# Optimization experiments

Measured on AMD Instinct MI355X. Metric: run time of the kernel, lower is better.

## Reference

```python
import jax, jax.numpy as jnp
import numpy as np

N = 100000        # nodes in the batched graph
E = 1_600_000     # directed edges
G = 256           # graphs in the batch
IN, H = 3, 64
EPS = 1e-5        # BatchNorm eps (eval mode: running stats, dropout off)


def setup_inputs() -> dict:
    key = jax.random.key(0)
    ks = jax.random.split(key, 40)
    inp = {}
    inp["x"] = jax.random.normal(ks[0], (N, IN), jnp.float32)
    inp["edge_index"] = jax.random.randint(ks[1], (2, E), 0, N, dtype=jnp.int32)
    inp["batch_idx"] = jnp.sort(jax.random.randint(ks[2], (N,), 0, G, dtype=jnp.int32))
    dims = [IN, H, H, H]  # zip(dims[:-1], dims[1:]) -> 3 GCN layers (as in source)
    k = 3
    for i in range(3):
        inp[f"W{i}"] = jax.random.normal(ks[k], (dims[i], dims[i + 1]), jnp.float32) * 0.1; k += 1
        inp[f"b{i}"] = jax.random.normal(ks[k], (dims[i + 1],), jnp.float32) * 0.01; k += 1
        inp[f"g{i}"] = jax.random.uniform(ks[k], (dims[i + 1],), jnp.float32, 0.5, 1.5); k += 1
        inp[f"be{i}"] = jax.random.normal(ks[k], (dims[i + 1],), jnp.float32) * 0.1; k += 1
        inp[f"rm{i}"] = jax.random.normal(ks[k], (dims[i + 1],), jnp.float32) * 0.1; k += 1
        inp[f"rv{i}"] = jax.random.uniform(ks[k], (dims[i + 1],), jnp.float32, 0.5, 1.5); k += 1
    inp["mW1"] = jax.random.normal(ks[k], (2 * H, 32), jnp.float32) * 0.1; k += 1
    inp["mb1"] = jnp.zeros((32,), jnp.float32)
    inp["mW2"] = jax.random.normal(ks[k], (32, 16), jnp.float32) * 0.1; k += 1
    inp["mb2"] = jnp.zeros((16,), jnp.float32)
    inp["mW3"] = jax.random.normal(ks[k], (16, 1), jnp.float32) * 0.1; k += 1
    inp["mb3"] = jnp.zeros((1,), jnp.float32)
    return inp


def _gcn(x, W, b, src, dst):
    # PyG GCNConv: add self-loops, symmetric D^-1/2 (A+I) D^-1/2 normalization
    h = x @ W                                   # [N, out]
    deg = jnp.zeros((N,), h.dtype).at[dst].add(1.0) + 1.0  # +1 self-loop
    dinv = jax.lax.rsqrt(deg)
    coef = dinv[src] * dinv[dst]                # [E]
    agg = jax.ops.segment_sum(h[src] * coef[:, None], dst, num_segments=N)
    agg = agg + h * (dinv * dinv)[:, None]      # self-loop message
    return agg + b


def _bn(x, g, be, rm, rv):
    return (x - rm) * jax.lax.rsqrt(rv + EPS) * g + be


def _forward(x, edge_index, batch_idx,
             W0, b0, g0, be0, rm0, rv0,
             W1, b1, g1, be1, rm1, rv1,
             W2, b2, g2, be2, rm2, rv2,
             mW1, mb1, mW2, mb2, mW3, mb3):
    src, dst = edge_index[0], edge_index[1]
    layers = [(W0, b0, g0, be0, rm0, rv0), (W1, b1, g1, be1, rm1, rv1), (W2, b2, g2, be2, rm2, rv2)]
    for (W, b, g, be, rm, rv) in layers:
        x = jax.nn.relu(_bn(_gcn(x, W, b, src, dst), g, be, rm, rv))
    cnt = jax.ops.segment_sum(jnp.ones((N,), x.dtype), batch_idx, num_segments=G)
    x_mean = jax.ops.segment_sum(x, batch_idx, num_segments=G) / jnp.maximum(cnt, 1.0)[:, None]
    x_max = jax.ops.segment_max(x, batch_idx, num_segments=G)
    x_max = jnp.where(jnp.isfinite(x_max), x_max, 0.0)
    xg = jnp.concatenate([x_mean, x_max], axis=1)  # [G, 2H]
    h = jax.nn.relu(xg @ mW1 + mb1)
    h = jax.nn.relu(h @ mW2 + mb2)
    return h @ mW3 + mb3                            # [G, 1]


def reference(x, edge_index, batch_idx,
              W0, b0, g0, be0, rm0, rv0,
              W1, b1, g1, be1, rm1, rv1,
              W2, b2, g2, be2, rm2, rv2,
              mW1, mb1, mW2, mb2, mW3, mb3):
    return _forward(x, edge_index, batch_idx,
                    W0, b0, g0, be0, rm0, rv0,
                    W1, b1, g1, be1, rm1, rv1,
                    W2, b2, g2, be2, rm2, rv2,
                    mW1, mb1, mW2, mb2, mW3, mb3)
```

## Files before the change

### kernel.cpp

```cpp
#include <hip/hip_runtime.h>
#include <hip/hip_fp16.h>

#define NN 100000
#define EE 1600000
#define GG 256
#define EPS 1e-5f
#define KB2 ((NN + 511) >> 9)
#define BCAP 10240
#define EPB 4096
#define EBLK ((EE + EPB - 1) / EPB)
#define NB256 ((NN + 255) / 256)

__device__ __forceinline__ unsigned int pack2(float x, float y) {
  __half2 h = __float22half2_rn(make_float2(x, y));
  return *reinterpret_cast<unsigned int*>(&h);
}
__device__ __forceinline__ uint2 pack4(float x, float y, float z, float w) {
  uint2 r;
  r.x = pack2(x, y);
  r.y = pack2(z, w);
  return r;
}
__device__ __forceinline__ void add8(float4& a0, float4& a1, uint4 v) {
  __half2 h0 = *reinterpret_cast<__half2*>(&v.x);
  __half2 h1 = *reinterpret_cast<__half2*>(&v.y);
  __half2 h2 = *reinterpret_cast<__half2*>(&v.z);
  __half2 h3 = *reinterpret_cast<__half2*>(&v.w);
  float2 f0 = __half22float2(h0), f1 = __half22float2(h1);
  float2 f2 = __half22float2(h2), f3 = __half22float2(h3);
  a0.x += f0.x; a0.y += f0.y; a0.z += f1.x; a0.w += f1.y;
  a1.x += f2.x; a1.y += f2.y; a1.z += f3.x; a1.w += f3.y;
}

__device__ __forceinline__ void gld16(uint4& d, const uint4* p) {
  asm volatile("global_load_dwordx4 %0, %1, off" : "=v"(d) : "v"(p));
}
__device__ __forceinline__ void gldf16(float4& d, const float4* p) {
  asm volatile("global_load_dwordx4 %0, %1, off" : "=v"(d) : "v"(p));
}

__global__ void k_passA(const int* __restrict__ ei, int* __restrict__ bfill,
                        int* __restrict__ tmp) {
  __shared__ int cnt[KB2], cur[KB2], base[KB2];
  int t = threadIdx.x;
  for (int b = t; b < KB2; b += 256) { cnt[b] = 0; cur[b] = 0; }
  __syncthreads();
  int e0 = blockIdx.x * EPB;
  int myb[16], myp[16];
#pragma unroll
  for (int j = 0; j < 16; ++j) {
    int e = e0 + j * 256 + t;
    int bb = -1, pp = 0;
    if (e < EE) {
      int ss = ei[e];
      int dd = ei[EE + e];
      bb = dd >> 9;
      pp = (ss << 9) | (dd & 511);
    }
    myb[j] = bb;
    myp[j] = pp;
    if (bb >= 0) atomicAdd(&cnt[bb], 1);
  }
  __syncthreads();
  for (int b = t; b < KB2; b += 256)
    if (cnt[b] > 0) base[b] = b * BCAP + atomicAdd(&bfill[b], cnt[b]);
  __syncthreads();
#pragma unroll
  for (int j = 0; j < 16; ++j) {
    int bb = myb[j];
    if (bb >= 0) {
      int slot = base[bb] + atomicAdd(&cur[bb], 1);
      tmp[slot] = myp[j];
    }
  }
}

__global__ void k_bucket(const int* __restrict__ tmp, const int* __restrict__ bfill,
                         const float* __restrict__ x, int* __restrict__ csr,
                         int* __restrict__ row, int* __restrict__ rowe,
                         float* __restrict__ dinv, float4* __restrict__ xd) {
  __shared__ int cnt[512], s[512], fillp[512];
  __shared__ int stmp[BCAP];
  int b = blockIdx.x, t = threadIdx.x;
  int nb = b << 9;
  int e0 = b * BCAP;
  int fill = bfill[b];
  cnt[t] = 0;
  cnt[t + 256] = 0;
  for (int e = t; e < fill; e += 256) stmp[e] = tmp[e0 + e];
  __syncthreads();
  for (int e = t; e < fill; e += 256) atomicAdd(&cnt[stmp[e] & 511], 1);
  __syncthreads();
  s[t] = cnt[t];
  s[t + 256] = cnt[t + 256];
  __syncthreads();
  for (int off = 1; off < 512; off <<= 1) {
    int i1 = t + 256;
    int v0 = (t >= off) ? s[t - off] : 0;
    int v1 = (i1 >= off) ? s[i1 - off] : 0;
    __syncthreads();
    s[t] += v0;
    s[i1] += v1;
    __syncthreads();
  }
#pragma unroll
  for (int k = 0; k < 2; ++k) {
    int i = t + k * 256;
    int excl = s[i] - cnt[i];
    fillp[i] = excl;
    int dst = nb + i;
    if (dst < NN) {
      row[dst] = e0 + excl;
      rowe[dst] = e0 + s[i];
      float d = rsqrtf((float)cnt[i] + 1.0f);
      dinv[dst] = d;
      xd[dst] = make_float4(x[dst * 3] * d, x[dst * 3 + 1] * d, x[dst * 3 + 2] * d, 0.f);
    }
  }
  __syncthreads();
  for (int e = t; e < fill; e += 256) {
    int ed = stmp[e];
    int slot = atomicAdd(&fillp[ed & 511], 1);
    csr[e0 + slot] = ed >> 9;
  }
}

__launch_bounds__(256, 4)
__global__ void k_agg3f(const float4* __restrict__ xd, const int* __restrict__ row,
                        const int* __restrict__ rowe, const int* __restrict__ csr,
                        const float* __restrict__ dinv,
                        const float* __restrict__ W, const float* __restrict__ b,
                        const float* __restrict__ gam, const float* __restrict__ bet,
                        const float* __restrict__ rm, const float* __restrict__ rv,
                        uint2* __restrict__ out) {
  int n = blockIdx.x * 256 + threadIdx.x;
  if (n >= NN) return;
  int s0 = row[n], s1 = rowe[n];
  float4 a = xd[n];
  float ax = a.x, ay = a.y, az = a.z;
  for (int i = s0; i < s1; i += 16) {
    int idx[16];
#pragma unroll
    for (int j = 0; j < 16; ++j) idx[j] = csr[min(i + j, s1 - 1)];
    float4 v[16];
#pragma unroll
    for (int j = 0; j < 16; ++j) gldf16(v[j], xd + idx[j]);
    asm volatile("s_waitcnt vmcnt(0)" ::: "memory");
    __builtin_amdgcn_sched_barrier(0);
    int rem = s1 - i;
#pragma unroll
    for (int j = 0; j < 16; ++j)
      if (j < rem) { ax += v[j].x; ay += v[j].y; az += v[j].z; }
  }
  float d = dinv[n];
  float t0 = ax * d, t1 = ay * d, t2 = az * d;
  const float4* W4 = (const float4*)W;
  const float4* b4 = (const float4*)b;
  const float4* g4p = (const float4*)gam;
  const float4* be4p = (const float4*)bet;
  const float4* rm4p = (const float4*)rm;
  const float4* rv4p = (const float4*)rv;
#pragma unroll
  for (int c4 = 0; c4 < 16; ++c4) {
    float4 w0 = W4[c4], w1 = W4[16 + c4], w2 = W4[32 + c4];
    float4 bb = b4[c4], g4 = g4p[c4], be4 = be4p[c4], rm4 = rm4p[c4], rv4 = rv4p[c4];
    float4 o;
    o.x = fmaf(t0, w0.x, fmaf(t1, w1.x, fmaf(t2, w2.x, bb.x)));
    o.y = fmaf(t0, w0.y, fmaf(t1, w1.y, fmaf(t2, w2.y, bb.y)));
    o.z = fmaf(t0, w0.z, fmaf(t1, w1.z, fmaf(t2, w2.z, bb.z)));
    o.w = fmaf(t0, w0.w, fmaf(t1, w1.w, fmaf(t2, w2.w, bb.w)));
    float scx = g4.x * rsqrtf(rv4.x + EPS), shx = be4.x - rm4.x * scx;
    float scy = g4.y * rsqrtf(rv4.y + EPS), shy = be4.y - rm4.y * scy;
    float scz = g4.z * rsqrtf(rv4.z + EPS), shz = be4.z - rm4.z * scz;
    float scw = g4.w * rsqrtf(rv4.w + EPS), shw = be4.w - rm4.w * scw;
    o.x = fmaxf(fmaf(o.x, scx, shx), 0.f) * d;
    o.y = fmaxf(fmaf(o.y, scy, shy), 0.f) * d;
    o.z = fmaxf(fmaf(o.z, scz, shz), 0.f) * d;
    o.w = fmaxf(fmaf(o.w, scw, shw), 0.f) * d;
    out[(size_t)n * 16 + c4] = pack4(o.x, o.y, o.z, o.w);
  }
}

template <bool MID>
__launch_bounds__(256, 4)
__global__ void k_layer2(const uint4* __restrict__ xs, const int* __restrict__ row,
                         const int* __restrict__ rowe, const int* __restrict__ csr,
                         const float* __restrict__ dinv,
                         const float* __restrict__ W, const float* __restrict__ b,
                         const float* __restrict__ gam, const float* __restrict__ bet,
                         const float* __restrict__ rm, const float* __restrict__ rv,
                         uint4* __restrict__ outv) {
  __shared__ float sh[32][68];
  int t = blockIdx.x * 256 + threadIdx.x;
  int n = t >> 3, sub = t & 7;
  int local = threadIdx.x >> 3;
  int s0 = row[n], s1 = rowe[n];
  float4 a0 = make_float4(0.f, 0.f, 0.f, 0.f);
  float4 a1 = make_float4(0.f, 0.f, 0.f, 0.f);
  add8(a0, a1, xs[(size_t)n * 8 + sub]);
  if (s0 < s1) {
    int e = s0 + sub;
    int myidx = (e < s1) ? csr[e] : n;
    for (int i = s0; i < s1; i += 8) {
      int e2 = i + 8 + sub;
      int pre = csr[min(e2, s1 - 1)];
      uint4 v0, v1, v2, v3, v4, v5, v6, v7;
      gld16(v0, xs + ((size_t)__shfl(myidx, 0, 8) * 8 + sub));
      gld16(v1, xs + ((size_t)__shfl(myidx, 1, 8) * 8 + sub));
      gld16(v2, xs + ((size_t)__shfl(myidx, 2, 8) * 8 + sub));
      gld16(v3, xs + ((size_t)__shfl(myidx, 3, 8) * 8 + sub));
      gld16(v4, xs + ((size_t)__shfl(myidx, 4, 8) * 8 + sub));
      gld16(v5, xs + ((size_t)__shfl(myidx, 5, 8) * 8 + sub));
      gld16(v6, xs + ((size_t)__shfl(myidx, 6, 8) * 8 + sub));
      gld16(v7, xs + ((size_t)__shfl(myidx, 7, 8) * 8 + sub));
      asm volatile("s_waitcnt vmcnt(0)" ::: "memory");
      __builtin_amdgcn_sched_barrier(0);
      int rem = s1 - i;
      add8(a0, a1, v0);
      if (rem > 1) add8(a0, a1, v1);
      if (rem > 2) add8(a0, a1, v2);
      if (rem > 3) add8(a0, a1, v3);
      if (rem > 4) add8(a0, a1, v4);
      if (rem > 5) add8(a0, a1, v5);
      if (rem > 6) add8(a0, a1, v6);
      if (rem > 7) add8(a0, a1, v7);
      myidx = (e2 < s1) ? pre : n;
    }
  }
  float d = dinv[n];
  float4 w0 = make_float4(a0.x * d, a0.y * d, a0.z * d, a0.w * d);
  float4 w1 = make_float4(a1.x * d, a1.y * d, a1.z * d, a1.w * d);
  *(float4*)&sh[local][sub * 8] = w0;
  *(float4*)&sh[local][sub * 8 + 4] = w1;
  __syncthreads();
  const float4* W4 = (const float4*)W;
  float4 accA = ((const float4*)b)[sub * 2];
  float4 accB = ((const float4*)b)[sub * 2 + 1];
#pragma unroll 8
  for (int k = 0; k < 64; ++k) {
    float xv = sh[local][k];
    float4 wA = W4[k * 16 + sub * 2];
    float4 wB = W4[k * 16 + sub * 2 + 1];
    accA.x = fmaf(xv, wA.x, accA.x);
    accA.y = fmaf(xv, wA.y, accA.y);
    accA.z = fmaf(xv, wA.z, accA.z);
    accA.w = fmaf(xv, wA.w, accA.w);
    accB.x = fmaf(xv, wB.x, accB.x);
    accB.y = fmaf(xv, wB.y, accB.y);
    accB.z = fmaf(xv, wB.z, accB.z);
    accB.w = fmaf(xv, wB.w, accB.w);
  }
  float4 gA = ((const float4*)gam)[sub * 2], gB = ((const float4*)gam)[sub * 2 + 1];
  float4 beA = ((const float4*)bet)[sub * 2], beB = ((const float4*)bet)[sub * 2 + 1];
  float4 rmA = ((const float4*)rm)[sub * 2], rmB = ((const float4*)rm)[sub * 2 + 1];
  float4 rvA = ((const float4*)rv)[sub * 2], rvB = ((const float4*)rv)[sub * 2 + 1];
  float4 oA, oB;
  {
    float sc = gA.x * rsqrtf(rvA.x + EPS); oA.x = fmaxf(fmaf(accA.x, sc, beA.x - rmA.x * sc), 0.f);
    sc = gA.y * rsqrtf(rvA.y + EPS); oA.y = fmaxf(fmaf(accA.y, sc, beA.y - rmA.y * sc), 0.f);
    sc = gA.z * rsqrtf(rvA.z + EPS); oA.z = fmaxf(fmaf(accA.z, sc, beA.z - rmA.z * sc), 0.f);
    sc = gA.w * rsqrtf(rvA.w + EPS); oA.w = fmaxf(fmaf(accA.w, sc, beA.w - rmA.w * sc), 0.f);
    sc = gB.x * rsqrtf(rvB.x + EPS); oB.x = fmaxf(fmaf(accB.x, sc, beB.x - rmB.x * sc), 0.f);
    sc = gB.y * rsqrtf(rvB.y + EPS); oB.y = fmaxf(fmaf(accB.y, sc, beB.y - rmB.y * sc), 0.f);
    sc = gB.z * rsqrtf(rvB.z + EPS); oB.z = fmaxf(fmaf(accB.z, sc, beB.z - rmB.z * sc), 0.f);
    sc = gB.w * rsqrtf(rvB.w + EPS); oB.w = fmaxf(fmaf(accB.w, sc, beB.w - rmB.w * sc), 0.f);
  }
  uint4 r;
  if (MID) {
    r.x = pack2(oA.x * d, oA.y * d);
    r.y = pack2(oA.z * d, oA.w * d);
    r.z = pack2(oB.x * d, oB.y * d);
    r.w = pack2(oB.z * d, oB.w * d);
  } else {
    r.x = pack2(oA.x, oA.y);
    r.y = pack2(oA.z, oA.w);
    r.z = pack2(oB.x, oB.y);
    r.w = pack2(oB.z, oB.w);
  }
  outv[(size_t)n * 8 + sub] = r;
}

__device__ __forceinline__ int lower_bound(const int* __restrict__ b, int target) {
  int lo = 0, hi = NN;
  while (lo < hi) {
    int m = (lo + hi) >> 1;
    if (b[m] < target) lo = m + 1; else hi = m;
  }
  return lo;
}

__global__ void k_poolmlp(const uint2* __restrict__ feat, const int* __restrict__ bidx,
                          const float* __restrict__ mW1, const float* __restrict__ mb1,
                          const float* __restrict__ mW2, const float* __restrict__ mb2,
                          const float* __restrict__ mW3, const float* __restrict__ mb3,
                          float* __restrict__ out) {
  __shared__ float4 shs[64][17], shm[64][17];
  __shared__ float xg[128], h1[32], h2[16];
  int g = blockIdx.x, t = threadIdx.x;
  int c4 = t & 15, r = t >> 4;
  int lo = lower_bound(bidx, g);
  int hi = lower_bound(bidx, g + 1);
  float4 s = make_float4(0.f, 0.f, 0.f, 0.f);
  float4 m = make_float4(0.f, 0.f, 0.f, 0.f);
  for (int i = lo + r; i < hi; i += 64) {
    uint2 u = feat[(size_t)i * 16 + c4];
    __half2 h0 = *reinterpret_cast<__half2*>(&u.x);
    __half2 h1v = *reinterpret_cast<__half2*>(&u.y);
    float2 f0 = __half22float2(h0), f1 = __half22float2(h1v);
    s.x += f0.x; s.y += f0.y; s.z += f1.x; s.w += f1.y;
    m.x = fmaxf(m.x, f0.x); m.y = fmaxf(m.y, f0.y);
    m.z = fmaxf(m.z, f1.x); m.w = fmaxf(m.w, f1.y);
  }
  shs[r][c4] = s;
  shm[r][c4] = m;
  __syncthreads();
  if (t < 16) {
    float4 cs = shs[0][t], cm = shm[0][t];
#pragma unroll
    for (int r2 = 1; r2 < 64; ++r2) {
      float4 as = shs[r2][t], am = shm[r2][t];
      cs.x += as.x; cs.y += as.y; cs.z += as.z; cs.w += as.w;
      cm.x = fmaxf(cm.x, am.x); cm.y = fmaxf(cm.y, am.y);
      cm.z = fmaxf(cm.z, am.z); cm.w = fmaxf(cm.w, am.w);
    }
    float inv = 1.0f / fmaxf((float)(hi - lo), 1.0f);
    xg[t * 4 + 0] = cs.x * inv; xg[t * 4 + 1] = cs.y * inv;
    xg[t * 4 + 2] = cs.z * inv; xg[t * 4 + 3] = cs.w * inv;
    xg[64 + t * 4 + 0] = cm.x; xg[64 + t * 4 + 1] = cm.y;
    xg[64 + t * 4 + 2] = cm.z; xg[64 + t * 4 + 3] = cm.w;
  }
  __syncthreads();
  if (t < 32) {
    float a = mb1[t];
    for (int k = 0; k < 128; ++k) a = fmaf(xg[k], mW1[k * 32 + t], a);
    h1[t] = fmaxf(a, 0.f);
  }
  __syncthreads();
  if (t < 16) {
    float a = mb2[t];
    for (int k = 0; k < 32; ++k) a = fmaf(h1[k], mW2[k * 16 + t], a);
    h2[t] = fmaxf(a, 0.f);
  }
  __syncthreads();
  if (t == 0) {
    float a = mb3[0];
    for (int k = 0; k < 16; ++k) a = fmaf(h2[k], mW3[k], a);
    out[g] = a;
  }
}

extern "C" void kernel_launch(void* const* d_in, const int* in_sizes, int n_in,
                              void* d_out, int out_size, void* d_ws, size_t ws_size,
                              hipStream_t stream) {
  const float* x = (const float*)d_in[0];
  const int* ei = (const int*)d_in[1];
  const int* bidx = (const int*)d_in[2];
  const float *W[3], *b[3], *gam[3], *bet[3], *rm[3], *rv[3];
  for (int l = 0; l < 3; ++l) {
    W[l] = (const float*)d_in[3 + 6 * l];
    b[l] = (const float*)d_in[4 + 6 * l];
    gam[l] = (const float*)d_in[5 + 6 * l];
    bet[l] = (const float*)d_in[6 + 6 * l];
    rm[l] = (const float*)d_in[7 + 6 * l];
    rv[l] = (const float*)d_in[8 + 6 * l];
  }
  const float* mW1 = (const float*)d_in[21];
  const float* mb1 = (const float*)d_in[22];
  const float* mW2 = (const float*)d_in[23];
  const float* mb2 = (const float*)d_in[24];
  const float* mW3 = (const float*)d_in[25];
  const float* mb3 = (const float*)d_in[26];
  float* out = (float*)d_out;

  char* ws = (char*)d_ws;
  size_t off = 0;
  auto alloc = [&](size_t bytes) {
    void* p = ws + off;
    off = (off + bytes + 1023) & ~(size_t)1023;
    return p;
  };
  float* dinv = (float*)alloc(NN * 4);
  int* row = (int*)alloc(NN * 4);
  int* rowe = (int*)alloc(NN * 4);
  int* csr = (int*)alloc((size_t)KB2 * BCAP * 4);
  int* bfill = (int*)alloc(256 * 4);
  float4* xd = (float4*)alloc((size_t)NN * 16);
  float* bufA = (float*)alloc((size_t)NN * 64 * 4);
  float* bufB = (float*)alloc((size_t)NN * 64 * 2);
  int* tmp = (int*)bufA;

  hipMemsetAsync(bfill, 0, 256 * 4, stream);

  k_passA<<<EBLK, 256, 0, stream>>>(ei, bfill, tmp);
  k_bucket<<<KB2, 256, 0, stream>>>(tmp, bfill, x, csr, row, rowe, dinv, xd);

  int nb8 = (NN * 8) / 256;

  k_agg3f<<<NB256, 256, 0, stream>>>(xd, row, rowe, csr, dinv, W[0], b[0], gam[0], bet[0],
                                     rm[0], rv[0], (uint2*)bufA);
  k_layer2<true><<<nb8, 256, 0, stream>>>((const uint4*)bufA, row, rowe, csr, dinv, W[1], b[1],
                                          gam[1], bet[1], rm[1], rv[1], (uint4*)bufB);
  k_layer2<false><<<nb8, 256, 0, stream>>>((const uint4*)bufB, row, rowe, csr, dinv, W[2], b[2],
                                           gam[2], bet[2], rm[2], rv[2], (uint4*)bufA);
  k_poolmlp<<<GG, 1024, 0, stream>>>((const uint2*)bufA, bidx, mW1, mb1, mW2, mb2, mW3, mb3, out);
}
```

Baseline: 320.5 us.

## Build CSR with global count/scan/scatter and fuse pooling into last layer

Replaces the two-pass bucketed CSR build (shared-memory per-bucket sort) with a global per-node degree count, a two-level prefix scan, and an atomic scatter into a compact CSR. It also moves the mean/max graph pooling into the final GCN layer's epilogue via shared-memory staging and global atomics, so the pooled kernel reduces to a small MLP. The scatter uses global atomics per edge, which makes CSR order nondeterministic and may contend, and the fused pooling adds atomic traffic to the last layer while no longer storing its output.

```diff
diff --git a/kernel.cpp b/kernel.cpp
--- a/kernel.cpp
+++ b/kernel.cpp
@@ -6,7 +6,6 @@
 #define GG 256
 #define EPS 1e-5f
 #define KB2 ((NN + 511) >> 9)
-#define BCAP 10240
 #define EPB 4096
 #define EBLK ((EE + EPB - 1) / EPB)
 #define NB256 ((NN + 255) / 256)
@@ -39,89 +38,79 @@
   asm volatile("global_load_dwordx4 %0, %1, off" : "=v"(d) : "v"(p));
 }
 
-__global__ void k_passA(const int* __restrict__ ei, int* __restrict__ bfill,
-                        int* __restrict__ tmp) {
-  __shared__ int cnt[KB2], cur[KB2], base[KB2];
+__global__ void k_cnt(const int* __restrict__ ei, int* __restrict__ cnt) {
+  int e0 = blockIdx.x * EPB;
   int t = threadIdx.x;
-  for (int b = t; b < KB2; b += 256) { cnt[b] = 0; cur[b] = 0; }
-  __syncthreads();
-  int e0 = blockIdx.x * EPB;
-  int myb[16], myp[16];
 #pragma unroll
   for (int j = 0; j < 16; ++j) {
     int e = e0 + j * 256 + t;
-    int bb = -1, pp = 0;
+    if (e < EE) atomicAdd(&cnt[ei[EE + e]], 1);
+  }
+}
+
+__global__ void k_scanA(const int* __restrict__ cnt, const float* __restrict__ x,
+                        int* __restrict__ rowloc, int* __restrict__ bsum,
+                        float* __restrict__ dinv, float4* __restrict__ xd) {
+  __shared__ int s[512];
+  int b = blockIdx.x, t = threadIdx.x;
+  int n = (b << 9) + t;
+  int c = (n < NN) ? cnt[n] : 0;
+  s[t] = c;
+  __syncthreads();
+  for (int off = 1; off < 512; off <<= 1) {
+    int v = (t >= off) ? s[t - off] : 0;
+    __syncthreads();
+    s[t] += v;
+    __syncthreads();
+  }
+  if (n < NN) {
+    rowloc[n] = s[t] - c;
+    float d = rsqrtf((float)c + 1.0f);
+    dinv[n] = d;
+    xd[n] = make_float4(x[n * 3] * d, x[n * 3 + 1] * d, x[n * 3 + 2] * d, 0.f);
+  }
+  if (t == 511) bsum[b] = s[t];
+}
+
+__global__ void k_scanB(const int* __restrict__ bsum, int* __restrict__ bbase) {
+  __shared__ int s[256];
+  int t = threadIdx.x;
+  int v = (t < KB2) ? bsum[t] : 0;
+  s[t] = v;
+  __syncthreads();
+  for (int off = 1; off < 256; off <<= 1) {
+    int add = (t >= off) ? s[t - off] : 0;
+    __syncthreads();
+    s[t] += add;
+    __syncthreads();
+  }
+  if (t < KB2) bbase[t] = s[t] - v;
+}
+
+__global__ void k_row(const int* __restrict__ rowloc, const int* __restrict__ cnt,
+                      const int* __restrict__ bbase, int* __restrict__ row,
+                      int* __restrict__ rowe, int* __restrict__ fill) {
+  int n = blockIdx.x * 256 + threadIdx.x;
+  if (n >= NN) return;
+  int r = rowloc[n] + bbase[n >> 9];
+  row[n] = r;
+  fill[n] = r;
+  rowe[n] = r + cnt[n];
+}
+
+__global__ void k_scatter(const int* __restrict__ ei, int* __restrict__ fill,
+                          int* __restrict__ csr) {
+  int e0 = blockIdx.x * EPB;
+  int t = threadIdx.x;
+#pragma unroll
+  for (int j = 0; j < 16; ++j) {
+    int e = e0 + j * 256 + t;
     if (e < EE) {
       int ss = ei[e];
       int dd = ei[EE + e];
-      bb = dd >> 9;
-      pp = (ss << 9) | (dd & 511);
+      int pos = atomicAdd(&fill[dd], 1);
+      csr[pos] = ss;
     }
-    myb[j] = bb;
-    myp[j] = pp;
-    if (bb >= 0) atomicAdd(&cnt[bb], 1);
-  }
-  __syncthreads();
-  for (int b = t; b < KB2; b += 256)
-    if (cnt[b] > 0) base[b] = b * BCAP + atomicAdd(&bfill[b], cnt[b]);
-  __syncthreads();
-#pragma unroll
-  for (int j = 0; j < 16; ++j) {
-    int bb = myb[j];
-    if (bb >= 0) {
-      int slot = base[bb] + atomicAdd(&cur[bb], 1);
-      tmp[slot] = myp[j];
-    }
-  }
-}
-
-__global__ void k_bucket(const int* __restrict__ tmp, const int* __restrict__ bfill,
-                         const float* __restrict__ x, int* __restrict__ csr,
-                         int* __restrict__ row, int* __restrict__ rowe,
-                         float* __restrict__ dinv, float4* __restrict__ xd) {
-  __shared__ int cnt[512], s[512], fillp[512];
-  __shared__ int stmp[BCAP];
-  int b = blockIdx.x, t = threadIdx.x;
-  int nb = b << 9;
-  int e0 = b * BCAP;
-  int fill = bfill[b];
-  cnt[t] = 0;
-  cnt[t + 256] = 0;
-  for (int e = t; e < fill; e += 256) stmp[e] = tmp[e0 + e];
-  __syncthreads();
-  for (int e = t; e < fill; e += 256) atomicAdd(&cnt[stmp[e] & 511], 1);
-  __syncthreads();
-  s[t] = cnt[t];
-  s[t + 256] = cnt[t + 256];
-  __syncthreads();
-  for (int off = 1; off < 512; off <<= 1) {
-    int i1 = t + 256;
-    int v0 = (t >= off) ? s[t - off] : 0;
-    int v1 = (i1 >= off) ? s[i1 - off] : 0;
-    __syncthreads();
-    s[t] += v0;
-    s[i1] += v1;
-    __syncthreads();
-  }
-#pragma unroll
-  for (int k = 0; k < 2; ++k) {
-    int i = t + k * 256;
-    int excl = s[i] - cnt[i];
-    fillp[i] = excl;
-    int dst = nb + i;
-    if (dst < NN) {
-      row[dst] = e0 + excl;
-      rowe[dst] = e0 + s[i];
-      float d = rsqrtf((float)cnt[i] + 1.0f);
-      dinv[dst] = d;
-      xd[dst] = make_float4(x[dst * 3] * d, x[dst * 3 + 1] * d, x[dst * 3 + 2] * d, 0.f);
-    }
-  }
-  __syncthreads();
-  for (int e = t; e < fill; e += 256) {
-    int ed = stmp[e];
-    int slot = atomicAdd(&fillp[ed & 511], 1);
-    csr[e0 + slot] = ed >> 9;
   }
 }
 
@@ -189,7 +178,8 @@
                          const float* __restrict__ W, const float* __restrict__ b,
                          const float* __restrict__ gam, const float* __restrict__ bet,
                          const float* __restrict__ rm, const float* __restrict__ rv,
-                         uint4* __restrict__ outv) {
+                         uint4* __restrict__ outv, const int* __restrict__ bidx,
+                         float* __restrict__ xsum, unsigned* __restrict__ xmaxu) {
   __shared__ float sh[32][68];
   int t = blockIdx.x * 256 + threadIdx.x;
   int n = t >> 3, sub = t & 7;
@@ -265,19 +255,37 @@
     sc = gB.z * rsqrtf(rvB.z + EPS); oB.z = fmaxf(fmaf(accB.z, sc, beB.z - rmB.z * sc), 0.f);
     sc = gB.w * rsqrtf(rvB.w + EPS); oB.w = fmaxf(fmaf(accB.w, sc, beB.w - rmB.w * sc), 0.f);
   }
-  uint4 r;
   if (MID) {
+    uint4 r;
     r.x = pack2(oA.x * d, oA.y * d);
     r.y = pack2(oA.z * d, oA.w * d);
     r.z = pack2(oB.x * d, oB.y * d);
     r.w = pack2(oB.z * d, oB.w * d);
+    outv[(size_t)n * 8 + sub] = r;
   } else {
-    r.x = pack2(oA.x, oA.y);
-    r.y = pack2(oA.z, oA.w);
-    r.z = pack2(oB.x, oB.y);
-    r.w = pack2(oB.z, oB.w);
-  }
-  outv[(size_t)n * 8 + sub] = r;
+    __syncthreads();
+    *(float4*)&sh[local][sub * 8] = oA;
+    *(float4*)&sh[local][sub * 8 + 4] = oB;
+    __syncthreads();
+    int c = threadIdx.x & 63, q = threadIdx.x >> 6;
+    int nb = blockIdx.x * 32 + q * 8;
+    float ps = 0.f, pm = 0.f;
+    int curg = bidx[nb];
+#pragma unroll
+    for (int r2 = 0; r2 < 8; ++r2) {
+      int g = bidx[nb + r2];
+      if (g != curg) {
+        atomicAdd(&xsum[(size_t)curg * 64 + c], ps);
+        atomicMax(&xmaxu[(size_t)curg * 64 + c], __float_as_uint(pm));
+        ps = 0.f; pm = 0.f; curg = g;
+      }
+      float v = sh[q * 8 + r2][c];
+      ps += v;
+      pm = fmaxf(pm, v);
+    }
+    atomicAdd(&xsum[(size_t)curg * 64 + c], ps);
+    atomicMax(&xmaxu[(size_t)curg * 64 + c], __float_as_uint(pm));
+  }
 }
 
 __device__ __forceinline__ int lower_bound(const int* __restrict__ b, int target) {
@@ -289,46 +297,19 @@
   return lo;
 }
 
-__global__ void k_poolmlp(const uint2* __restrict__ feat, const int* __restrict__ bidx,
-                          const float* __restrict__ mW1, const float* __restrict__ mb1,
-                          const float* __restrict__ mW2, const float* __restrict__ mb2,
-                          const float* __restrict__ mW3, const float* __restrict__ mb3,
-                          float* __restrict__ out) {
-  __shared__ float4 shs[64][17], shm[64][17];
+__global__ void k_mlp(const float* __restrict__ xsum, const float* __restrict__ xmaxf,
+                      const int* __restrict__ bidx,
+                      const float* __restrict__ mW1, const float* __restrict__ mb1,
+                      const float* __restrict__ mW2, const float* __restrict__ mb2,
+                      const float* __restrict__ mW3, const float* __restrict__ mb3,
+                      float* __restrict__ out) {
   __shared__ float xg[128], h1[32], h2[16];
   int g = blockIdx.x, t = threadIdx.x;
-  int c4 = t & 15, r = t >> 4;
   int lo = lower_bound(bidx, g);
   int hi = lower_bound(bidx, g + 1);
-  float4 s = make_float4(0.f, 0.f, 0.f, 0.f);
-  float4 m = make_float4(0.f, 0.f, 0.f, 0.f);
-  for (int i = lo + r; i < hi; i += 64) {
-    uint2 u = feat[(size_t)i * 16 + c4];
-    __half2 h0 = *reinterpret_cast<__half2*>(&u.x);
-    __half2 h1v = *reinterpret_cast<__half2*>(&u.y);
-    float2 f0 = __half22float2(h0), f1 = __half22float2(h1v);
-    s.x += f0.x; s.y += f0.y; s.z += f1.x; s.w += f1.y;
-    m.x = fmaxf(m.x, f0.x); m.y = fmaxf(m.y, f0.y);
-    m.z = fmaxf(m.z, f1.x); m.w = fmaxf(m.w, f1.y);
-  }
-  shs[r][c4] = s;
-  shm[r][c4] = m;
-  __syncthreads();
-  if (t < 16) {
-    float4 cs = shs[0][t], cm = shm[0][t];
-#pragma unroll
-    for (int r2 = 1; r2 < 64; ++r2) {
-      float4 as = shs[r2][t], am = shm[r2][t];
-      cs.x += as.x; cs.y += as.y; cs.z += as.z; cs.w += as.w;
-      cm.x = fmaxf(cm.x, am.x); cm.y = fmaxf(cm.y, am.y);
-      cm.z = fmaxf(cm.z, am.z); cm.w = fmaxf(cm.w, am.w);
-    }
-    float inv = 1.0f / fmaxf((float)(hi - lo), 1.0f);
-    xg[t * 4 + 0] = cs.x * inv; xg[t * 4 + 1] = cs.y * inv;
-    xg[t * 4 + 2] = cs.z * inv; xg[t * 4 + 3] = cs.w * inv;
-    xg[64 + t * 4 + 0] = cm.x; xg[64 + t * 4 + 1] = cm.y;
-    xg[64 + t * 4 + 2] = cm.z; xg[64 + t * 4 + 3] = cm.w;
-  }
+  float inv = 1.0f / fmaxf((float)(hi - lo), 1.0f);
+  xg[t] = xsum[(size_t)g * 64 + t] * inv;
+  xg[64 + t] = xmaxf[(size_t)g * 64 + t];
   __syncthreads();
   if (t < 32) {
     float a = mb1[t];
@@ -382,25 +363,38 @@
   float* dinv = (float*)alloc(NN * 4);
   int* row = (int*)alloc(NN * 4);
   int* rowe = (int*)alloc(NN * 4);
-  int* csr = (int*)alloc((size_t)KB2 * BCAP * 4);
-  int* bfill = (int*)alloc(256 * 4);
+  int* cnt = (int*)alloc(NN * 4);
+  int* rowloc = (int*)alloc(NN * 4);
+  int* fill = (int*)alloc(NN * 4);
+  int* bsum = (int*)alloc(256 * 4);
+  int* bbase = (int*)alloc(256 * 4);
+  int* csr = (int*)alloc((size_t)EE * 4);
   float4* xd = (float4*)alloc((size_t)NN * 16);
-  float* bufA = (float*)alloc((size_t)NN * 64 * 4);
+  float* pool = (float*)alloc(GG * 64 * 4 * 2);
+  float* xsum = pool;
+  unsigned* xmaxu = (unsigned*)(pool + GG * 64);
+  float* bufA = (float*)alloc((size_t)NN * 64 * 2);
   float* bufB = (float*)alloc((size_t)NN * 64 * 2);
-  int* tmp = (int*)bufA;
-
-  hipMemsetAsync(bfill, 0, 256 * 4, stream);
-
-  k_passA<<<EBLK, 256, 0, stream>>>(ei, bfill, tmp);
-  k_bucket<<<KB2, 256, 0, stream>>>(tmp, bfill, x, csr, row, rowe, dinv, xd);
+
+  hipMemsetAsync(cnt, 0, NN * 4, stream);
+  hipMemsetAsync(pool, 0, GG * 64 * 4 * 2, stream);
+
+  k_cnt<<<EBLK, 256, 0, stream>>>(ei, cnt);
+  k_scanA<<<KB2, 512, 0, stream>>>(cnt, x, rowloc, bsum, dinv, xd);
+  k_scanB<<<1, 256, 0, stream>>>(bsum, bbase);
+  k_row<<<NB256, 256, 0, stream>>>(rowloc, cnt, bbase, row, rowe, fill);
+  k_scatter<<<EBLK, 256, 0, stream>>>(ei, fill, csr);
 
   int nb8 = (NN * 8) / 256;
 
   k_agg3f<<<NB256, 256, 0, stream>>>(xd, row, rowe, csr, dinv, W[0], b[0], gam[0], bet[0],
                                      rm[0], rv[0], (uint2*)bufA);
   k_layer2<true><<<nb8, 256, 0, stream>>>((const uint4*)bufA, row, rowe, csr, dinv, W[1], b[1],
-                                          gam[1], bet[1], rm[1], rv[1], (uint4*)bufB);
+                                          gam[1], bet[1], rm[1], rv[1], (uint4*)bufB,
+                                          bidx, xsum, xmaxu);
   k_layer2<false><<<nb8, 256, 0, stream>>>((const uint4*)bufB, row, rowe, csr, dinv, W[2], b[2],
-                                           gam[2], bet[2], rm[2], rv[2], (uint4*)bufA);
-  k_poolmlp<<<GG, 1024, 0, stream>>>((const uint2*)bufA, bidx, mW1, mb1, mW2, mb2, mW3, mb3, out);
-}
+                                           gam[2], bet[2], rm[2], rv[2], (uint4*)bufA,
+                                           bidx, xsum, xmaxu);
+  k_mlp<<<GG, 64, 0, stream>>>(xsum, (const float*)xmaxu, bidx, mW1, mb1, mW2, mb2,
+                               mW3, mb3, out);
+}
```

Measured after the change: 479.5 us. 1.5x slower.
